# Optimization experiments

Hardware: AMD Instinct MI355X
Metric: run time of the kernel (lower is better)

Reference implementation:

```python
import jax, jax.numpy as jnp
import numpy as np

ALPHA = 0.2
BN_EPS = 1e-5
NEG = -9e15


def make_quaternion_mul(kernel):
    # kernel: [in/4, out]; split columns into quaternion components
    dim = kernel.shape[1] // 4
    r, i, j, k = jnp.split(kernel, 4, axis=1)
    r2 = jnp.concatenate([r, -i, -j, -k], axis=0)
    i2 = jnp.concatenate([i, r, -k, j], axis=0)
    j2 = jnp.concatenate([j, k, r, -i], axis=0)
    k2 = jnp.concatenate([k, -j, i, r], axis=0)
    return jnp.concatenate([r2, i2, j2, k2], axis=1)  # [in, out]


def setup_inputs() -> dict:
    key = jax.random.key(0)
    k1, k2, k3, k4 = jax.random.split(key, 4)
    N, IN, OUT = 8192, 512, 128
    inp = jax.random.normal(k1, (N, IN), dtype=jnp.float32)
    adj = jax.random.randint(k2, (N, N), 0, 2, dtype=jnp.int32)
    # xavier-like init for params
    W = jax.random.normal(k3, (IN // 4, OUT), dtype=jnp.float32) * (1.0 / np.sqrt(IN // 4))
    a = jax.random.normal(k4, (2 * OUT, 1), dtype=jnp.float32) * (1.0 / np.sqrt(2 * OUT))
    bn_gamma = jnp.ones((OUT,), dtype=jnp.float32)
    bn_beta = jnp.zeros((OUT,), dtype=jnp.float32)
    return {"input": inp, "adj": adj, "W": W, "a": a, "bn_gamma": bn_gamma, "bn_beta": bn_beta}


def reference(input, adj, W, a, bn_gamma, bn_beta):
    out_features = W.shape[1]
    hamilton = make_quaternion_mul(W)           # [in, out]
    h = input @ hamilton                        # [N, out]
    # a_input[i,j] = concat(h_i, h_j); a_input @ a decomposes as
    # (h @ a1)_i + (h @ a2)_j with a1 = a[:out], a2 = a[out:]
    a1 = a[:out_features, 0]                    # [out]
    a2 = a[out_features:, 0]                    # [out]
    s1 = h @ a1                                 # [N]
    s2 = h @ a2                                 # [N]
    e = s1[:, None] + s2[None, :]               # [N, N]
    e = jnp.where(e > 0, e, ALPHA * e)          # leaky_relu
    attention = jnp.where(adj > 0, e, NEG)
    attention = jax.nn.softmax(attention, axis=1)
    # dropout is identity in inference
    h_prime = attention @ h                     # [N, out]
    # BatchNorm1d (training-mode batch statistics, biased variance)
    mean = jnp.mean(h_prime, axis=0)
    var = jnp.var(h_prime, axis=0)
    h_prime = (h_prime - mean) / jnp.sqrt(var + BN_EPS) * bn_gamma + bn_beta
    # concat=True -> ELU
    return jax.nn.elu(h_prime)
```

## Files before the change

### kernel.cpp

```cpp
#include <hip/hip_runtime.h>
#include <hip/hip_bf16.h>
#include <math.h>

#define N_NODES 8192
#define IN_F    512
#define OUT_F   128
#define LRELU_A 0.2f
#define EPS_BN  1e-5f
#define MSH     40.0f
#define NSPLIT  8
#define JSPAN   (N_NODES / NSPLIT)
#define TILE_I  64
#define HSTR    72
#define ASTR    36
#define MSTR    34

typedef unsigned short u16;
typedef unsigned int   u32;
typedef unsigned long long u64;
typedef __attribute__((ext_vector_type(8))) short  short8;
typedef __attribute__((ext_vector_type(4))) float  floatx4;

__device__ __forceinline__ u16 f2bf_rtn(float x) {
    u32 u = __float_as_uint(x);
    return (u16)((u + 0x7fffu + ((u >> 16) & 1u)) >> 16);
}

__global__ __launch_bounds__(256) void k_hamT(const float* __restrict__ W, u16* __restrict__ hamT,
                                              float* __restrict__ s1, float* __restrict__ s2,
                                              float* __restrict__ cs, float* __restrict__ cq) {
    const int idx = blockIdx.x * 256 + threadIdx.x;
    if (idx < N_NODES) { s1[idx] = 0.f; s2[idx] = 0.f; }
    if (idx < OUT_F)   { cs[idx] = 0.f; cq[idx] = 0.f; }
    const int c = idx >> 9, k = idx & 511;
    const int b = c >> 5, cc = c & 31, p = k >> 7, q = k & 127;
    const u32 NEGMASK = 0x284Eu;
    const float sg = ((NEGMASK >> (b * 4 + p)) & 1u) ? -1.f : 1.f;
    hamT[idx] = f2bf_rtn(sg * W[q * 128 + (b ^ p) * 32 + cc]);
}

__global__ __launch_bounds__(256) void k_h(const float* __restrict__ inp, const u16* __restrict__ hamT,
                                           const float* __restrict__ a,
                                           u16* __restrict__ hT, float* __restrict__ s1, float* __restrict__ s2) {
    __shared__ float inA[2][64 * ASTR];
    const int t = threadIdx.x;
    const int lane = t & 63, wid = t >> 6;
    const int quad = lane >> 4, n = lane & 15;
    const int i0 = blockIdx.x * 64;
    const int chalf = blockIdx.y;
    const int srow = t >> 2, scol = (t & 3) * 8;

    {
        const float* sp = inp + (size_t)(i0 + srow) * IN_F + scol;
        *(float4*)&inA[0][srow * ASTR + scol]     = *(const float4*)sp;
        *(float4*)&inA[0][srow * ASTR + scol + 4] = *(const float4*)(sp + 4);
    }
    __syncthreads();

    floatx4 acc[4];
#pragma unroll
    for (int ct = 0; ct < 4; ct++) acc[ct] = (floatx4){0.f, 0.f, 0.f, 0.f};

#pragma unroll 2
    for (int kk = 0; kk < 16; ++kk) {
        const int cur = kk & 1;
        float4 f0n, f1n;
        const bool more = (kk + 1 < 16);
        if (more) {
            const float* sp = inp + (size_t)(i0 + srow) * IN_F + (kk + 1) * 32 + scol;
            f0n = *(const float4*)sp;
            f1n = *(const float4*)(sp + 4);
        }
        float4 a0 = *(const float4*)&inA[cur][(wid * 16 + n) * ASTR + quad * 8];
        float4 a1 = *(const float4*)&inA[cur][(wid * 16 + n) * ASTR + quad * 8 + 4];
        union { u32 u[4]; short8 s; } fa;
        fa.u[0] = (u32)f2bf_rtn(a0.x) | ((u32)f2bf_rtn(a0.y) << 16);
        fa.u[1] = (u32)f2bf_rtn(a0.z) | ((u32)f2bf_rtn(a0.w) << 16);
        fa.u[2] = (u32)f2bf_rtn(a1.x) | ((u32)f2bf_rtn(a1.y) << 16);
        fa.u[3] = (u32)f2bf_rtn(a1.z) | ((u32)f2bf_rtn(a1.w) << 16);
#pragma unroll
        for (int ct = 0; ct < 4; ++ct) {
            short8 fb = *(const short8*)&hamT[(chalf * 64 + ct * 16 + n) * IN_F + kk * 32 + quad * 8];
            acc[ct] = __builtin_amdgcn_mfma_f32_16x16x32_bf16(fa.s, fb, acc[ct], 0, 0, 0);
        }
        if (more) {
            *(float4*)&inA[cur ^ 1][srow * ASTR + scol]     = f0n;
            *(float4*)&inA[cur ^ 1][srow * ASTR + scol + 4] = f1n;
        }
        __syncthreads();
    }

    const int iw = i0 + wid * 16;
#pragma unroll
    for (int ct = 0; ct < 4; ++ct) {
        const int c = chalf * 64 + ct * 16 + n;
        u64 pk = (u64)f2bf_rtn(acc[ct][0])
               | ((u64)f2bf_rtn(acc[ct][1]) << 16)
               | ((u64)f2bf_rtn(acc[ct][2]) << 32)
               | ((u64)f2bf_rtn(acc[ct][3]) << 48);
        *(u64*)&hT[(size_t)c * N_NODES + iw + quad * 4] = pk;
    }

    float p1[4] = {0.f, 0.f, 0.f, 0.f}, p2[4] = {0.f, 0.f, 0.f, 0.f};
#pragma unroll
    for (int ct = 0; ct < 4; ++ct) {
        const int c = chalf * 64 + ct * 16 + n;
        const float a1v = a[c], a2v = a[OUT_F + c];
#pragma unroll
        for (int r = 0; r < 4; ++r) { p1[r] += acc[ct][r] * a1v; p2[r] += acc[ct][r] * a2v; }
    }
#pragma unroll
    for (int m = 1; m < 16; m <<= 1) {
#pragma unroll
        for (int r = 0; r < 4; ++r) {
            p1[r] += __shfl_xor(p1[r], m, 64);
            p2[r] += __shfl_xor(p2[r], m, 64);
        }
    }
    if (n == 0) {
#pragma unroll
        for (int r = 0; r < 4; ++r) {
            atomicAdd(&s1[iw + quad * 4 + r], p1[r]);
            atomicAdd(&s2[iw + quad * 4 + r], p2[r]);
        }
    }
}

__global__ __launch_bounds__(256, 3) void k_att(const int* __restrict__ adj, const u16* __restrict__ hT,
                                                const float* __restrict__ s1, const float* __restrict__ s2,
                                                float* __restrict__ Opart, float* __restrict__ Lpart) {
    __shared__ u16 hs[2][128 * HSTR];
    __shared__ float s2s[JSPAN];
    __shared__ u32 mk[64 * MSTR];
    const int t = threadIdx.x;
    const int lane = t & 63, wid = t >> 6;
    const int quad = lane >> 4, n = lane & 15;
    const int i0 = blockIdx.x * TILE_I;
    const int jbase = blockIdx.y * JSPAN;
    const int i_lane = i0 + wid * 16 + n;
    const float s1v = s1[i_lane];
    const int scr = t >> 3, scj = (t & 7) * 8;

    *(float4*)&s2s[t * 4] = *(const float4*)&s2[jbase + t * 4];

    {
        const size_t rowbase = (size_t)(i0 + wid * 16);
#pragma unroll
        for (int rb = 0; rb < 4; ++rb) {
            uint4 v[4][4];
#pragma unroll
            for (int r = 0; r < 4; ++r) {
                const int* ap = adj + (rowbase + rb * 4 + r) * N_NODES + jbase + lane * 4;
#pragma unroll
                for (int g = 0; g < 4; ++g) v[r][g] = *(const uint4*)(ap + g * 256);
            }
#pragma unroll
            for (int r = 0; r < 4; ++r) {
                u32* mp = &mk[(wid * 16 + rb * 4 + r) * MSTR];
#pragma unroll
                for (int g = 0; g < 4; ++g) {
                    u64 c0 = __ballot((int)v[r][g].x > 0);
                    u64 c1 = __ballot((int)v[r][g].y > 0);
                    u64 c2 = __ballot((int)v[r][g].z > 0);
                    u64 c3 = __ballot((int)v[r][g].w > 0);
                    if (lane < 4) {
                        u64 val = (lane == 0) ? c0 : (lane == 1) ? c1 : (lane == 2) ? c2 : c3;
                        *(u64*)&mp[g * 8 + lane * 2] = val;
                    }
                }
            }
        }
    }

#pragma unroll
    for (int ps = 0; ps < 4; ++ps) {
        const int cr = ps * 32 + scr;
        uint4 v = *(const uint4*)&hT[(size_t)cr * N_NODES + jbase + scj];
        *(uint4*)&hs[0][cr * HSTR + scj] = v;
    }
    __syncthreads();

    u32 m8[8];
    {
        const u32* mp = &mk[(wid * 16 + n) * MSTR];
#pragma unroll
        for (int w = 0; w < 8; ++w) m8[w] = mp[w];
    }

    floatx4 acc[8];
#pragma unroll
    for (int ct = 0; ct < 8; ct++) acc[ct] = (floatx4){0.f, 0.f, 0.f, 0.f};
    float Lacc = 0.f;

#pragma unroll 4
    for (int ch = 0; ch < 16; ++ch) {
        const int cur = ch & 1;
        const bool more = (ch + 1 < 16);
        uint4 H[4];
        if (more) {
#pragma unroll
            for (int ps = 0; ps < 4; ++ps) {
                const int cr = ps * 32 + scr;
                H[ps] = *(const uint4*)&hT[(size_t)cr * N_NODES + jbase + (ch + 1) * 64 + scj];
            }
        }
        u32 m8n[8];
#pragma unroll
        for (int w = 0; w < 8; ++w) m8n[w] = m8[w];
        if ((ch & 3) == 3 && more) {
            const u32* mp = &mk[(wid * 16 + n) * MSTR + ((ch >> 2) + 1) * 8];
#pragma unroll
            for (int w = 0; w < 8; ++w) m8n[w] = mp[w];
        }

        short8 fa[2];
#pragma unroll
        for (int ks = 0; ks < 2; ++ks) {
            const int jl = ch * 64 + ks * 32 + quad * 8;
            float4 sa = *(const float4*)&s2s[jl];
            float4 sb = *(const float4*)&s2s[jl + 4];
            const float sv[8] = {sa.x, sa.y, sa.z, sa.w, sb.x, sb.y, sb.z, sb.w};
            union { u32 u[4]; short8 s; } cv;
#pragma unroll
            for (int jh = 0; jh < 4; ++jh) {
                float w2[2];
#pragma unroll
                for (int e = 0; e < 2; ++e) {
                    const int jj = jh * 2 + e;
                    const u32 word = m8[(jj & 3) * 2 + ((ch >> 1) & 1)];
                    const int sh = (ch & 1) * 16 + ks * 8 + quad * 2 + (jj >> 2);
                    const u32 mbit = (word >> sh) & 1u;
                    float sc = s1v + sv[jj];
                    sc = fmaxf(sc, LRELU_A * sc);
                    float w = mbit ? __expf(sc - MSH) : 0.f;
                    Lacc += w;
                    w2[e] = w;
                }
                cv.u[jh] = (u32)f2bf_rtn(w2[0]) | ((u32)f2bf_rtn(w2[1]) << 16);
            }
            fa[ks] = cv.s;
        }
#pragma unroll
        for (int ct = 0; ct < 8; ++ct) {
            const int boff = (ct * 16 + n) * HSTR;
            short8 fb0 = *(const short8*)&hs[cur][boff + quad * 8];
            short8 fb1 = *(const short8*)&hs[cur][boff + 32 + quad * 8];
            acc[ct] = __builtin_amdgcn_mfma_f32_16x16x32_bf16(fa[0], fb0, acc[ct], 0, 0, 0);
            acc[ct] = __builtin_amdgcn_mfma_f32_16x16x32_bf16(fa[1], fb1, acc[ct], 0, 0, 0);
        }
        if (more) {
#pragma unroll
            for (int ps = 0; ps < 4; ++ps) {
                const int cr = ps * 32 + scr;
                *(uint4*)&hs[cur ^ 1][cr * HSTR + scj] = H[ps];
            }
        }
        __syncthreads();
#pragma unroll
        for (int w = 0; w < 8; ++w) m8[w] = m8n[w];
    }

    Lacc += __shfl_xor(Lacc, 16, 64);
    Lacc += __shfl_xor(Lacc, 32, 64);
    if (lane < 16)
        Lpart[(size_t)blockIdx.y * N_NODES + i_lane] = Lacc;

    const size_t obase = (size_t)blockIdx.y * N_NODES * OUT_F;
#pragma unroll
    for (int ct = 0; ct < 8; ++ct) {
#pragma unroll
        for (int r = 0; r < 4; ++r) {
            const int i = i0 + wid * 16 + quad * 4 + r;
            Opart[obase + (size_t)i * OUT_F + ct * 16 + n] = acc[ct][r];
        }
    }
}

__global__ __launch_bounds__(256) void k_comb(const float* __restrict__ Opart, const float* __restrict__ Lpart,
                                              float* __restrict__ hp, float* __restrict__ cs, float* __restrict__ cq) {
    const int t = threadIdx.x;
    const int c = t & 127, half = t >> 7;
    const int ibase = blockIdx.x * 16;
    float sv = 0.f, sq = 0.f;
    for (int k = 0; k < 8; k++) {
        const int i = ibase + half + (k << 1);
        float o = 0.f, L = 0.f;
#pragma unroll
        for (int s = 0; s < NSPLIT; s++) {
            o += Opart[((size_t)s * N_NODES + i) * OUT_F + c];
            L += Lpart[(size_t)s * N_NODES + i];
        }
        float v = L > 0.f ? o / L : 0.f;
        hp[(size_t)i * OUT_F + c] = v;
        sv += v; sq += v * v;
    }
    __shared__ float red[256];
    red[t] = sv; __syncthreads();
    if (half == 0) atomicAdd(&cs[c], sv + red[t + 128]);
    __syncthreads(); red[t] = sq; __syncthreads();
    if (half == 0) atomicAdd(&cq[c], sq + red[t + 128]);
}

__global__ __launch_bounds__(256) void k_bn(const float* __restrict__ hp, const float* __restrict__ cs,
                                            const float* __restrict__ cq, const float* __restrict__ gamma,
                                            const float* __restrict__ beta, float* __restrict__ out) {
    const int idx = blockIdx.x * 256 + threadIdx.x;
    const int c = idx & 127;
    const float mean = cs[c] * (1.f / N_NODES);
    const float var  = cq[c] * (1.f / N_NODES) - mean * mean;
    float x = (hp[idx] - mean) * rsqrtf(var + EPS_BN) * gamma[c] + beta[c];
    x = x > 0.f ? x : expm1f(x);
    out[idx] = x;
}

extern "C" void kernel_launch(void* const* d_in, const int* in_sizes, int n_in,
                              void* d_out, int out_size, void* d_ws, size_t ws_size,
                              hipStream_t stream) {
    (void)in_sizes; (void)n_in; (void)out_size; (void)ws_size;
    const float* inp   = (const float*)d_in[0];
    const int*   adj   = (const int*)d_in[1];
    const float* W     = (const float*)d_in[2];
    const float* a     = (const float*)d_in[3];
    const float* gamma = (const float*)d_in[4];
    const float* beta  = (const float*)d_in[5];
    float* out = (float*)d_out;

    char* wsb = (char*)d_ws;
    u16*   hamT = (u16*)wsb;   wsb += (size_t)OUT_F * IN_F * 2;
    u16*   hT   = (u16*)wsb;   wsb += (size_t)OUT_F * N_NODES * 2;
    float* s1   = (float*)wsb; wsb += N_NODES * 4;
    float* s2   = (float*)wsb; wsb += N_NODES * 4;
    float* Op   = (float*)wsb; wsb += (size_t)NSPLIT * N_NODES * OUT_F * 4;
    float* Lp   = (float*)wsb; wsb += (size_t)NSPLIT * N_NODES * 4;
    float* hp   = (float*)wsb; wsb += (size_t)N_NODES * OUT_F * 4;
    float* cs   = (float*)wsb; wsb += OUT_F * 4;
    float* cq   = (float*)wsb; wsb += OUT_F * 4;

    hipLaunchKernelGGL(k_hamT, dim3(256), dim3(256), 0, stream, W, hamT, s1, s2, cs, cq);
    hipLaunchKernelGGL(k_h,    dim3(128, 2), dim3(256), 0, stream, inp, hamT, a, hT, s1, s2);
    hipLaunchKernelGGL(k_att,  dim3(128, NSPLIT), dim3(256), 0, stream, adj, hT, s1, s2, Op, Lp);
    hipLaunchKernelGGL(k_comb, dim3(512), dim3(256), 0, stream, Op, Lp, hp, cs, cq);
    hipLaunchKernelGGL(k_bn,   dim3(4096), dim3(256), 0, stream, hp, cs, cq, gamma, beta, out);
}
```

Before: 484.8 us.

## Load hT MFMA operands directly from global memory, dropping LDS double buffer

Removes the shared-memory double buffer for the transposed h tile and its per-chunk __syncthreads, so each wave loads its bf16 B-fragments straight from global/L2 into registers right before the MFMAs. Mask words are now read from LDS once per group of four chunks. This cuts LDS footprint and block-wide barriers, which may raise occupancy and remove sync stalls. The cost is redundant global loads of hT across the four waves, and per-thread 16-byte loads strided by N_NODES rows, with no explicit prefetch to hide their latency.

```diff
diff --git a/kernel.cpp b/kernel.cpp
--- a/kernel.cpp
+++ b/kernel.cpp
@@ -11,7 +11,6 @@
 #define NSPLIT  8
 #define JSPAN   (N_NODES / NSPLIT)
 #define TILE_I  64
-#define HSTR    72
 #define ASTR    36
 #define MSTR    34
 
@@ -129,7 +128,6 @@
 __global__ __launch_bounds__(256, 3) void k_att(const int* __restrict__ adj, const u16* __restrict__ hT,
                                                 const float* __restrict__ s1, const float* __restrict__ s2,
                                                 float* __restrict__ Opart, float* __restrict__ Lpart) {
-    __shared__ u16 hs[2][128 * HSTR];
     __shared__ float s2s[JSPAN];
     __shared__ u32 mk[64 * MSTR];
     const int t = threadIdx.x;
@@ -139,7 +137,6 @@
     const int jbase = blockIdx.y * JSPAN;
     const int i_lane = i0 + wid * 16 + n;
     const float s1v = s1[i_lane];
-    const int scr = t >> 3, scj = (t & 7) * 8;
 
     *(float4*)&s2s[t * 4] = *(const float4*)&s2[jbase + t * 4];
 
@@ -171,93 +168,64 @@
             }
         }
     }
-
-#pragma unroll
-    for (int ps = 0; ps < 4; ++ps) {
-        const int cr = ps * 32 + scr;
-        uint4 v = *(const uint4*)&hT[(size_t)cr * N_NODES + jbase + scj];
-        *(uint4*)&hs[0][cr * HSTR + scj] = v;
-    }
     __syncthreads();
 
-    u32 m8[8];
-    {
-        const u32* mp = &mk[(wid * 16 + n) * MSTR];
-#pragma unroll
-        for (int w = 0; w < 8; ++w) m8[w] = mp[w];
-    }
+    const u32* mrow = &mk[(wid * 16 + n) * MSTR];
+    const u16* hrow = hT + (size_t)n * N_NODES + jbase + quad * 8;
 
     floatx4 acc[8];
 #pragma unroll
     for (int ct = 0; ct < 8; ct++) acc[ct] = (floatx4){0.f, 0.f, 0.f, 0.f};
     float Lacc = 0.f;
 
-#pragma unroll 4
-    for (int ch = 0; ch < 16; ++ch) {
-        const int cur = ch & 1;
-        const bool more = (ch + 1 < 16);
-        uint4 H[4];
-        if (more) {
-#pragma unroll
-            for (int ps = 0; ps < 4; ++ps) {
-                const int cr = ps * 32 + scr;
-                H[ps] = *(const uint4*)&hT[(size_t)cr * N_NODES + jbase + (ch + 1) * 64 + scj];
-            }
-        }
-        u32 m8n[8];
-#pragma unroll
-        for (int w = 0; w < 8; ++w) m8n[w] = m8[w];
-        if ((ch & 3) == 3 && more) {
-            const u32* mp = &mk[(wid * 16 + n) * MSTR + ((ch >> 2) + 1) * 8];
-#pragma unroll
-            for (int w = 0; w < 8; ++w) m8n[w] = mp[w];
-        }
-
-        short8 fa[2];
-#pragma unroll
-        for (int ks = 0; ks < 2; ++ks) {
-            const int jl = ch * 64 + ks * 32 + quad * 8;
-            float4 sa = *(const float4*)&s2s[jl];
-            float4 sb = *(const float4*)&s2s[jl + 4];
-            const float sv[8] = {sa.x, sa.y, sa.z, sa.w, sb.x, sb.y, sb.z, sb.w};
-            union { u32 u[4]; short8 s; } cv;
-#pragma unroll
-            for (int jh = 0; jh < 4; ++jh) {
-                float w2[2];
-#pragma unroll
-                for (int e = 0; e < 2; ++e) {
-                    const int jj = jh * 2 + e;
-                    const u32 word = m8[(jj & 3) * 2 + ((ch >> 1) & 1)];
-                    const int sh = (ch & 1) * 16 + ks * 8 + quad * 2 + (jj >> 2);
-                    const u32 mbit = (word >> sh) & 1u;
-                    float sc = s1v + sv[jj];
-                    sc = fmaxf(sc, LRELU_A * sc);
-                    float w = mbit ? __expf(sc - MSH) : 0.f;
-                    Lacc += w;
-                    w2[e] = w;
+#pragma unroll 1
+    for (int g = 0; g < 4; ++g) {
+        u32 m8[8];
+#pragma unroll
+        for (int w = 0; w < 8; ++w) m8[w] = mrow[g * 8 + w];
+#pragma unroll
+        for (int chi = 0; chi < 4; ++chi) {
+            const int ch = g * 4 + chi;
+            short8 fb0[8], fb1[8];
+#pragma unroll
+            for (int ct = 0; ct < 8; ++ct) {
+                const u16* hp_ = hrow + (size_t)(ct * 16) * N_NODES + ch * 64;
+                fb0[ct] = *(const short8*)hp_;
+                fb1[ct] = *(const short8*)(hp_ + 32);
+            }
+            short8 fa[2];
+#pragma unroll
+            for (int ks = 0; ks < 2; ++ks) {
+                const int jl = ch * 64 + ks * 32 + quad * 8;
+                float4 sa = *(const float4*)&s2s[jl];
+                float4 sb = *(const float4*)&s2s[jl + 4];
+                const float sv[8] = {sa.x, sa.y, sa.z, sa.w, sb.x, sb.y, sb.z, sb.w};
+                union { u32 u[4]; short8 s; } cv;
+#pragma unroll
+                for (int jh = 0; jh < 4; ++jh) {
+                    float w2[2];
+#pragma unroll
+                    for (int e = 0; e < 2; ++e) {
+                        const int jj = jh * 2 + e;
+                        const u32 word = m8[(jj & 3) * 2 + (chi >> 1)];
+                        const int sh = (chi & 1) * 16 + ks * 8 + quad * 2 + (jj >> 2);
+                        const u32 mbit = (word >> sh) & 1u;
+                        float sc = s1v + sv[jj];
+                        sc = fmaxf(sc, LRELU_A * sc);
+                        float w = mbit ? __expf(sc - MSH) : 0.f;
+                        Lacc += w;
+                        w2[e] = w;
+                    }
+                    cv.u[jh] = (u32)f2bf_rtn(w2[0]) | ((u32)f2bf_rtn(w2[1]) << 16);
                 }
-                cv.u[jh] = (u32)f2bf_rtn(w2[0]) | ((u32)f2bf_rtn(w2[1]) << 16);
-            }
-            fa[ks] = cv.s;
-        }
-#pragma unroll
-        for (int ct = 0; ct < 8; ++ct) {
-            const int boff = (ct * 16 + n) * HSTR;
-            short8 fb0 = *(const short8*)&hs[cur][boff + quad * 8];
-            short8 fb1 = *(const short8*)&hs[cur][boff + 32 + quad * 8];
-            acc[ct] = __builtin_amdgcn_mfma_f32_16x16x32_bf16(fa[0], fb0, acc[ct], 0, 0, 0);
-            acc[ct] = __builtin_amdgcn_mfma_f32_16x16x32_bf16(fa[1], fb1, acc[ct], 0, 0, 0);
-        }
-        if (more) {
-#pragma unroll
-            for (int ps = 0; ps < 4; ++ps) {
-                const int cr = ps * 32 + scr;
-                *(uint4*)&hs[cur ^ 1][cr * HSTR + scj] = H[ps];
-            }
-        }
-        __syncthreads();
-#pragma unroll
-        for (int w = 0; w < 8; ++w) m8[w] = m8n[w];
+                fa[ks] = cv.s;
+            }
+#pragma unroll
+            for (int ct = 0; ct < 8; ++ct) {
+                acc[ct] = __builtin_amdgcn_mfma_f32_16x16x32_bf16(fa[0], fb0[ct], acc[ct], 0, 0, 0);
+                acc[ct] = __builtin_amdgcn_mfma_f32_16x16x32_bf16(fa[1], fb1[ct], acc[ct], 0, 0, 0);
+            }
+        }
     }
 
     Lacc += __shfl_xor(Lacc, 16, 64);
```

Measured after the change: 569.1 us. 1.17x slower.
